# Performance work log

Hardware: AMD Instinct MI355X
Metric: run time of the kernel (lower is better)

Reference implementation:

```python
import jax, jax.numpy as jnp
import numpy as np

N_NODES = 100000
N_EDGES = 1600000
C_IN, C_HID, C_OUT = 32, 32, 8
N_AGENTS = 1000


def _glorot(key, shape):
    fan_in, fan_out = shape[0], shape[1]
    lim = float(np.sqrt(6.0 / (fan_in + fan_out)))
    return jax.random.uniform(key, shape, jnp.float32, -lim, lim)


def setup_inputs() -> dict:
    key = jax.random.key(0)
    ks = jax.random.split(key, 16)
    x = jax.random.normal(ks[0], (N_NODES, C_IN), jnp.float32)
    edge_index = jax.random.randint(ks[1], (2, N_EDGES), 0, N_NODES, jnp.int64)
    d = {"x": x, "edge_index": edge_index}
    dims = [(C_IN, C_HID), (C_HID, C_HID), (C_HID, C_HID)]
    for i, (di, do) in enumerate(dims, start=1):
        d[f"W_l{i}"] = _glorot(ks[2 * i], (di, do))        # neighbor (aggregated) weight
        d[f"b_l{i}"] = jnp.zeros((do,), jnp.float32)
        d[f"W_r{i}"] = _glorot(ks[2 * i + 1], (di, do))    # root/self weight (no bias)
    d["W_out"] = _glorot(ks[10], (C_HID, C_OUT))
    d["b_out"] = jnp.zeros((C_OUT,), jnp.float32)
    return d


def _sage_conv(x, src, dst, W_l, b_l, W_r):
    # mean-aggregate neighbor features at destination nodes
    msg = x[src]                                               # [E, d] gather
    summed = jax.ops.segment_sum(msg, dst, num_segments=N_NODES)
    cnt = jax.ops.segment_sum(jnp.ones((src.shape[0],), x.dtype), dst,
                              num_segments=N_NODES)
    agg = summed / jnp.maximum(cnt, 1.0)[:, None]              # deg==0 -> 0
    return agg @ W_l + b_l + x @ W_r


def reference(x, edge_index, W_l1, b_l1, W_r1, W_l2, b_l2, W_r2,
              W_l3, b_l3, W_r3, W_out, b_out):
    src, dst = edge_index[0], edge_index[1]
    h = jax.nn.relu(_sage_conv(x, src, dst, W_l1, b_l1, W_r1))
    h = jax.nn.relu(_sage_conv(h, src, dst, W_l2, b_l2, W_r2))
    h = jax.nn.relu(_sage_conv(h, src, dst, W_l3, b_l3, W_r3))
    out = h @ W_out + b_out
    return out[:N_AGENTS]
```

## Files before the change

kernel.cpp:

```cpp
#include <hip/hip_runtime.h>
#include <hip/hip_bf16.h>

#define N_NODES 100000
#define N_EDGES 1600000
#define N_AGENTS 1000

#define NB 782
#define ABLK 512
#define CHUNK (N_EDGES / ABLK)
#define CONV_BLOCKS 3125

typedef short s16x8 __attribute__((ext_vector_type(8)));
typedef float f32x4 __attribute__((ext_vector_type(4)));

__device__ __forceinline__ unsigned short f2bf(float f) {
    unsigned u = __float_as_uint(f);
    u += 0x7fffu + ((u >> 16) & 1u);
    return (unsigned short)(u >> 16);
}
__device__ __forceinline__ float bflo(unsigned u) { return __uint_as_float(u << 16); }
__device__ __forceinline__ float bfhi(unsigned u) { return __uint_as_float(u & 0xffff0000u); }

__global__ __launch_bounds__(256) void hist_prep_kernel(
    const int* __restrict__ dst, int* __restrict__ partialT,
    const float* __restrict__ x, unsigned short* __restrict__ xb,
    const float* __restrict__ Wl1, const float* __restrict__ Wr1,
    const float* __restrict__ Wl2, const float* __restrict__ Wr2,
    const float* __restrict__ Wl3, const float* __restrict__ Wr3,
    unsigned short* __restrict__ Wcat)
{
    int b = blockIdx.x;
    if (b < ABLK) {
        __shared__ int hist[NB];
        for (int i = threadIdx.x; i < NB; i += 256) hist[i] = 0;
        __syncthreads();
        int beg = b * CHUNK;
        for (int e = beg + threadIdx.x; e < beg + CHUNK; e += 256)
            atomicAdd(&hist[dst[e] >> 7], 1);
        __syncthreads();
        for (int i = threadIdx.x; i < NB; i += 256) partialT[i * ABLK + b] = hist[i];
    } else if (b < ABLK + CONV_BLOCKS) {
        int i = (b - ABLK) * 256 + threadIdx.x;
        float4 v = ((const float4*)x)[i];
        ((ushort4*)xb)[i] = make_ushort4(f2bf(v.x), f2bf(v.y), f2bf(v.z), f2bf(v.w));
    } else {
        int gid = (b - ABLK - CONV_BLOCKS) * 256 + threadIdx.x;
        if (gid >= 3 * 2048) return;
        int L = gid >> 11, idx = gid & 2047;
        int k = idx >> 5, n = idx & 31;
        const float* Wl = (L == 0) ? Wl1 : (L == 1) ? Wl2 : Wl3;
        const float* Wr = (L == 0) ? Wr1 : (L == 1) ? Wr2 : Wr3;
        float v = (k < 32) ? Wl[k * 32 + n] : Wr[(k - 32) * 32 + n];
        Wcat[gid] = f2bf(v);
    }
}

__global__ __launch_bounds__(256) void bucket_prefix_kernel(
    const int* __restrict__ partialT, int* __restrict__ baseT, int* __restrict__ tot)
{
    int wave = threadIdx.x >> 6, lane = threadIdx.x & 63;
    int t = blockIdx.x * 4 + wave;
    if (t >= NB) return;
    const int4* p = (const int4*)(partialT + (size_t)t * ABLK);
    int4 u0 = p[lane * 2], u1 = p[lane * 2 + 1];
    int v0 = u0.x, v1 = u0.y, v2 = u0.z, v3 = u0.w;
    int v4 = u1.x, v5 = u1.y, v6 = u1.z, v7 = u1.w;
    int p0 = 0, p1 = v0, p2 = p1 + v1, p3 = p2 + v2;
    int p4 = p3 + v3, p5 = p4 + v4, p6 = p5 + v5, p7 = p6 + v6;
    int s = p7 + v7;
    int x = s;
    #pragma unroll
    for (int off = 1; off < 64; off <<= 1) {
        int y = __shfl_up(x, off);
        if (lane >= off) x += y;
    }
    int excl = x - s;
    int4* q = (int4*)(baseT + (size_t)t * ABLK);
    q[lane * 2]     = make_int4(excl + p0, excl + p1, excl + p2, excl + p3);
    q[lane * 2 + 1] = make_int4(excl + p4, excl + p5, excl + p6, excl + p7);
    if (lane == 63) tot[t] = x;
}

__global__ __launch_bounds__(1024) void total_scan_kernel(
    const int* __restrict__ tot, int* __restrict__ bstart)
{
    __shared__ int tmp[1024];
    int t = threadIdx.x;
    int v = (t < NB) ? tot[t] : 0;
    tmp[t] = v;
    __syncthreads();
    for (int off = 1; off < 1024; off <<= 1) {
        int u = (t >= off) ? tmp[t - off] : 0;
        __syncthreads();
        tmp[t] += u;
        __syncthreads();
    }
    if (t < NB) {
        bstart[t] = tmp[t] - v;
        if (t == NB - 1) bstart[NB] = tmp[t];
    }
}

__global__ __launch_bounds__(256) void bucket_scatter_kernel(
    const int* __restrict__ src, const int* __restrict__ dst,
    const int* __restrict__ baseT, const int* __restrict__ bstart,
    int* __restrict__ ebuf)
{
    __shared__ int cur[NB];
    int b = blockIdx.x;
    for (int i = threadIdx.x; i < NB; i += 256)
        cur[i] = bstart[i] + baseT[(size_t)i * ABLK + b];
    __syncthreads();
    int beg = b * CHUNK;
    for (int e = beg + threadIdx.x; e < beg + CHUNK; e += 256) {
        int d = dst[e];
        int slot = atomicAdd(&cur[d >> 7], 1);
        ebuf[slot] = src[e] | ((d & 127) << 17);
    }
}

__global__ __launch_bounds__(256) void bucket_csr_kernel(
    const int* __restrict__ bstart, const int* __restrict__ ebuf,
    int* __restrict__ rowptr, float* __restrict__ inv, int* __restrict__ esrc)
{
    __shared__ int hist4[512], cur4[512], tmp[256];
    int b = blockIdx.x;
    int t = threadIdx.x;
    int beg = bstart[b], end = bstart[b + 1];
    hist4[t] = 0; hist4[t + 256] = 0;
    __syncthreads();
    for (int i = beg + t; i < end; i += 256) {
        int p = ebuf[i];
        int ln = (p >> 17) & 127;
        int cls = (p & 0x1FFFF) >> 15;
        atomicAdd(&hist4[ln * 4 + cls], 1);
    }
    __syncthreads();
    int c0 = 0, c1 = 0, c2 = 0, c3 = 0, v = 0;
    if (t < 128) {
        c0 = hist4[t * 4 + 0]; c1 = hist4[t * 4 + 1];
        c2 = hist4[t * 4 + 2]; c3 = hist4[t * 4 + 3];
        v = c0 + c1 + c2 + c3;
    }
    tmp[t] = v;
    __syncthreads();
    for (int off = 1; off < 256; off <<= 1) {
        int u = (t >= off) ? tmp[t - off] : 0;
        __syncthreads();
        tmp[t] += u;
        __syncthreads();
    }
    int excl = tmp[t] - v;
    int node = b * 128 + t;
    if (t < 128 && node < N_NODES) {
        int start = beg + excl;
        rowptr[node] = start;
        inv[node] = 1.0f / fmaxf((float)v, 1.0f);
        cur4[t * 4 + 0] = start;
        cur4[t * 4 + 1] = start + c0;
        cur4[t * 4 + 2] = start + c0 + c1;
        cur4[t * 4 + 3] = start + c0 + c1 + c2;
    }
    if (b == NB - 1 && t == 0) rowptr[N_NODES] = N_EDGES;
    __syncthreads();
    for (int i = beg + t; i < end; i += 256) {
        int p = ebuf[i];
        int ln = (p >> 17) & 127;
        int s = p & 0x1FFFF;
        int slot = atomicAdd(&cur4[ln * 4 + (s >> 15)], 1);
        esrc[slot] = s;
    }
}

__global__ __launch_bounds__(256) void sage_fused_kernel(
    const int* __restrict__ rowptr, const int* __restrict__ esrc,
    const float* __restrict__ inv, const unsigned short* __restrict__ hb,
    const unsigned short* __restrict__ Wcat, const float* __restrict__ bl,
    const float* __restrict__ Wout, const float* __restrict__ bout,
    void* __restrict__ outp, int n_nodes, int final)
{
    __shared__ unsigned short sW[2048];
    __shared__ float sb[32];
    __shared__ unsigned short smean[64 * 40];
    __shared__ float sh3[64 * 33];
    __shared__ float sWo[256];
    __shared__ float sbo[8];

    int tid = threadIdx.x;
    ((uint4*)sW)[tid] = ((const uint4*)Wcat)[tid];
    if (tid < 32) sb[tid] = bl[tid];
    if (final) {
        sWo[tid] = Wout[tid];
        if (tid < 8) sbo[tid] = bout[tid];
    }

    int lane = tid & 63, wave = tid >> 6;

    int g = lane >> 2, q = lane & 3;
    int nodeA = blockIdx.x * 64 + wave * 16 + g;
    int beg = 0, end = 0;
    if (nodeA < n_nodes) { beg = rowptr[nodeA]; end = rowptr[nodeA + 1]; }
    float a0 = 0.f, a1 = 0.f, a2 = 0.f, a3 = 0.f;
    float a4 = 0.f, a5 = 0.f, a6 = 0.f, a7 = 0.f;
    int j = beg;
    for (; j + 3 < end; j += 4) {
        int s0 = esrc[j];
        int s1 = esrc[j + 1];
        int s2 = esrc[j + 2];
        int s3 = esrc[j + 3];
        uint4 u0 = *(const uint4*)(hb + s0 * 32 + q * 8);
        uint4 u1 = *(const uint4*)(hb + s1 * 32 + q * 8);
        uint4 u2 = *(const uint4*)(hb + s2 * 32 + q * 8);
        uint4 u3 = *(const uint4*)(hb + s3 * 32 + q * 8);
        a0 += bflo(u0.x); a1 += bfhi(u0.x);
        a2 += bflo(u0.y); a3 += bfhi(u0.y);
        a4 += bflo(u0.z); a5 += bfhi(u0.z);
        a6 += bflo(u0.w); a7 += bfhi(u0.w);
        a0 += bflo(u1.x); a1 += bfhi(u1.x);
        a2 += bflo(u1.y); a3 += bfhi(u1.y);
        a4 += bflo(u1.z); a5 += bfhi(u1.z);
        a6 += bflo(u1.w); a7 += bfhi(u1.w);
        a0 += bflo(u2.x); a1 += bfhi(u2.x);
        a2 += bflo(u2.y); a3 += bfhi(u2.y);
        a4 += bflo(u2.z); a5 += bfhi(u2.z);
        a6 += bflo(u2.w); a7 += bfhi(u2.w);
        a0 += bflo(u3.x); a1 += bfhi(u3.x);
        a2 += bflo(u3.y); a3 += bfhi(u3.y);
        a4 += bflo(u3.z); a5 += bfhi(u3.z);
        a6 += bflo(u3.w); a7 += bfhi(u3.w);
    }
    for (; j < end; j++) {
        int s = esrc[j];
        uint4 u = *(const uint4*)(hb + s * 32 + q * 8);
        a0 += bflo(u.x); a1 += bfhi(u.x);
        a2 += bflo(u.y); a3 += bfhi(u.y);
        a4 += bflo(u.z); a5 += bfhi(u.z);
        a6 += bflo(u.w); a7 += bfhi(u.w);
    }
    float iv = (nodeA < n_nodes) ? inv[nodeA] : 0.f;
    uint4 o;
    o.x = (unsigned)f2bf(a0 * iv) | ((unsigned)f2bf(a1 * iv) << 16);
    o.y = (unsigned)f2bf(a2 * iv) | ((unsigned)f2bf(a3 * iv) << 16);
    o.z = (unsigned)f2bf(a4 * iv) | ((unsigned)f2bf(a5 * iv) << 16);
    o.w = (unsigned)f2bf(a6 * iv) | ((unsigned)f2bf(a7 * iv) << 16);
    int mrow = wave * 16 + g;
    *(uint4*)&smean[mrow * 40 + q * 8] = o;
    __syncthreads();

    int l15 = lane & 15, quad = lane >> 4;
    s16x8 bf_[2][2];
    #pragma unroll
    for (int kt = 0; kt < 2; kt++)
        #pragma unroll
        for (int nt = 0; nt < 2; nt++)
            #pragma unroll
            for (int jj = 0; jj < 8; jj++) {
                int k = kt * 32 + quad * 8 + jj;
                bf_[kt][nt][jj] = (short)sW[k * 32 + l15 + nt * 16];
            }
    float bias0 = sb[l15], bias1 = sb[l15 + 16];

    int tilebase = blockIdx.x * 64 + wave * 16;
    int nodeD = tilebase + l15;
    int na = min(nodeD, n_nodes - 1);
    s16x8 am = *(const s16x8*)&smean[(wave * 16 + l15) * 40 + quad * 8];
    s16x8 as = *(const s16x8*)(hb + (size_t)na * 32 + quad * 8);
    f32x4 acc0 = {0.f, 0.f, 0.f, 0.f};
    f32x4 acc1 = {0.f, 0.f, 0.f, 0.f};
    acc0 = __builtin_amdgcn_mfma_f32_16x16x32_bf16(am, bf_[0][0], acc0, 0, 0, 0);
    acc0 = __builtin_amdgcn_mfma_f32_16x16x32_bf16(as, bf_[1][0], acc0, 0, 0, 0);
    acc1 = __builtin_amdgcn_mfma_f32_16x16x32_bf16(am, bf_[0][1], acc1, 0, 0, 0);
    acc1 = __builtin_amdgcn_mfma_f32_16x16x32_bf16(as, bf_[1][1], acc1, 0, 0, 0);

    if (!final) {
        #pragma unroll
        for (int r = 0; r < 4; r++) {
            int onode = tilebase + quad * 4 + r;
            if (onode < n_nodes) {
                ((unsigned short*)outp)[onode * 32 + l15]      = f2bf(fmaxf(acc0[r] + bias0, 0.f));
                ((unsigned short*)outp)[onode * 32 + l15 + 16] = f2bf(fmaxf(acc1[r] + bias1, 0.f));
            }
        }
    } else {
        #pragma unroll
        for (int r = 0; r < 4; r++) {
            int row = wave * 16 + quad * 4 + r;
            sh3[row * 33 + l15]      = fmaxf(acc0[r] + bias0, 0.f);
            sh3[row * 33 + l15 + 16] = fmaxf(acc1[r] + bias1, 0.f);
        }
        __syncthreads();
        #pragma unroll
        for (int i = tid; i < 512; i += 256) {
            int ln = i >> 3, c = i & 7;
            int gn = blockIdx.x * 64 + ln;
            if (gn < N_AGENTS) {
                float ov = sbo[c];
                #pragma unroll
                for (int k = 0; k < 32; k++) ov += sh3[ln * 33 + k] * sWo[k * 8 + c];
                ((float*)outp)[gn * 8 + c] = ov;
            }
        }
    }
}

extern "C" void kernel_launch(void* const* d_in, const int* in_sizes, int n_in,
                              void* d_out, int out_size, void* d_ws, size_t ws_size,
                              hipStream_t stream) {
    const float* x   = (const float*)d_in[0];
    const int* ei    = (const int*)d_in[1];
    const float* Wl1 = (const float*)d_in[2];
    const float* bl1 = (const float*)d_in[3];
    const float* Wr1 = (const float*)d_in[4];
    const float* Wl2 = (const float*)d_in[5];
    const float* bl2 = (const float*)d_in[6];
    const float* Wr2 = (const float*)d_in[7];
    const float* Wl3 = (const float*)d_in[8];
    const float* bl3 = (const float*)d_in[9];
    const float* Wr3 = (const float*)d_in[10];
    const float* Wout = (const float*)d_in[11];
    const float* bout = (const float*)d_in[12];
    float* out = (float*)d_out;

    const int* src = ei;
    const int* dst = ei + N_EDGES;

    char* ws = (char*)d_ws;
    int*   rowptr   = (int*)ws;                                ws += (size_t)(N_NODES + 8) * 4;
    float* inv      = (float*)ws;                              ws += (size_t)N_NODES * 4;
    int*   partialT = (int*)ws;                                ws += (size_t)NB * ABLK * 4;
    int*   baseT    = (int*)ws;                                ws += (size_t)NB * ABLK * 4;
    int*   tot      = (int*)ws;                                ws += 784 * 4;
    int*   bstart   = (int*)ws;                                ws += 784 * 4;
    int*   esrc     = (int*)ws;                                ws += (size_t)N_EDGES * 4;
    unsigned short* hXb   = (unsigned short*)ws;               ws += (size_t)N_NODES * 32 * 2;
    unsigned short* hAb   = (unsigned short*)ws;               ws += (size_t)N_NODES * 32 * 2;
    unsigned short* hBb   = (unsigned short*)ws;               ws += (size_t)N_NODES * 32 * 2;
    unsigned short* Wcat  = (unsigned short*)ws;               ws += 3 * 2048 * 2;
    int*   ebuf     = (int*)hAb;

    hist_prep_kernel<<<ABLK + CONV_BLOCKS + 24, 256, 0, stream>>>(
        dst, partialT, x, hXb, Wl1, Wr1, Wl2, Wr2, Wl3, Wr3, Wcat);
    bucket_prefix_kernel<<<(NB + 3) / 4, 256, 0, stream>>>(partialT, baseT, tot);
    total_scan_kernel<<<1, 1024, 0, stream>>>(tot, bstart);
    bucket_scatter_kernel<<<ABLK, 256, 0, stream>>>(src, dst, baseT, bstart, ebuf);
    bucket_csr_kernel<<<NB, 256, 0, stream>>>(bstart, ebuf, rowptr, inv, esrc);

    sage_fused_kernel<<<(N_NODES + 63) / 64, 256, 0, stream>>>(
        rowptr, esrc, inv, hXb, Wcat, bl1, Wout, bout, hAb, N_NODES, 0);
    sage_fused_kernel<<<(N_NODES + 63) / 64, 256, 0, stream>>>(
        rowptr, esrc, inv, hAb, Wcat + 2048, bl2, Wout, bout, hBb, N_NODES, 0);
    sage_fused_kernel<<<(N_AGENTS + 63) / 64, 256, 0, stream>>>(
        rowptr, esrc, inv, hBb, Wcat + 4096, bl3, Wout, bout, out, N_AGENTS, 1);
}
```

Baseline: 200.0 us.

## Compute layer 2 only on nodes reachable from output agents

```diff
diff --git a/kernel.cpp b/kernel.cpp
--- a/kernel.cpp
+++ b/kernel.cpp
@@ -9,6 +9,9 @@
 #define ABLK 512
 #define CHUNK (N_EDGES / ABLK)
 #define CONV_BLOCKS 3125
+#define FLAGS_I4 25024
+#define FLAG_BLOCKS 98
+#define AGRID 280
 
 typedef short s16x8 __attribute__((ext_vector_type(8)));
 typedef float f32x4 __attribute__((ext_vector_type(4)));
@@ -27,7 +30,7 @@
     const float* __restrict__ Wl1, const float* __restrict__ Wr1,
     const float* __restrict__ Wl2, const float* __restrict__ Wr2,
     const float* __restrict__ Wl3, const float* __restrict__ Wr3,
-    unsigned short* __restrict__ Wcat)
+    unsigned short* __restrict__ Wcat, int* __restrict__ flags)
 {
     int b = blockIdx.x;
     if (b < ABLK) {
@@ -43,15 +46,17 @@
         int i = (b - ABLK) * 256 + threadIdx.x;
         float4 v = ((const float4*)x)[i];
         ((ushort4*)xb)[i] = make_ushort4(f2bf(v.x), f2bf(v.y), f2bf(v.z), f2bf(v.w));
-    } else {
+    } else if (b < ABLK + CONV_BLOCKS + 24) {
         int gid = (b - ABLK - CONV_BLOCKS) * 256 + threadIdx.x;
-        if (gid >= 3 * 2048) return;
         int L = gid >> 11, idx = gid & 2047;
         int k = idx >> 5, n = idx & 31;
         const float* Wl = (L == 0) ? Wl1 : (L == 1) ? Wl2 : Wl3;
         const float* Wr = (L == 0) ? Wr1 : (L == 1) ? Wr2 : Wr3;
         float v = (k < 32) ? Wl[k * 32 + n] : Wr[(k - 32) * 32 + n];
         Wcat[gid] = f2bf(v);
+    } else {
+        int gid = (b - ABLK - CONV_BLOCKS - 24) * 256 + threadIdx.x;
+        if (gid < FLAGS_I4) ((int4*)flags)[gid] = make_int4(0, 0, 0, 0);
     }
 }
 
@@ -170,6 +175,40 @@
         int slot = atomicAdd(&cur4[ln * 4 + (s >> 15)], 1);
         esrc[slot] = s;
     }
+}
+
+__global__ __launch_bounds__(256) void active_mark_kernel(
+    const int* __restrict__ rowptr, const int* __restrict__ esrc,
+    int* __restrict__ flags, int* __restrict__ acount)
+{
+    int gid = blockIdx.x * 256 + threadIdx.x;
+    if (gid == 0) *acount = 0;
+    if (gid < N_AGENTS) flags[gid] = 1;
+    int e1 = rowptr[N_AGENTS];
+    for (int j = gid; j < e1; j += gridDim.x * 256)
+        flags[esrc[j]] = 1;
+}
+
+__global__ __launch_bounds__(256) void active_compact_kernel(
+    const int* __restrict__ flags, int* __restrict__ alist, int* __restrict__ acount)
+{
+    int gid = blockIdx.x * 256 + threadIdx.x;
+    int f = (gid < N_NODES) ? flags[gid] : 0;
+    int lane = threadIdx.x & 63, wave = threadIdx.x >> 6;
+    unsigned long long m = __ballot(f != 0);
+    int pre = __popcll(m & ((1ull << lane) - 1ull));
+    __shared__ int wbase[4];
+    __shared__ int bbase;
+    if (lane == 0) wbase[wave] = __popcll(m);
+    __syncthreads();
+    if (threadIdx.x == 0) {
+        int t0 = wbase[0], t1 = t0 + wbase[1], t2 = t1 + wbase[2];
+        int tot = t2 + wbase[3];
+        bbase = atomicAdd(acount, tot);
+        wbase[0] = 0; wbase[1] = t0; wbase[2] = t1; wbase[3] = t2;
+    }
+    __syncthreads();
+    if (f) alist[bbase + wbase[wave] + pre] = gid;
 }
 
 __global__ __launch_bounds__(256) void sage_fused_kernel(
@@ -303,6 +342,118 @@
     }
 }
 
+__global__ __launch_bounds__(256) void sage_fused_act_kernel(
+    const int* __restrict__ rowptr, const int* __restrict__ esrc,
+    const float* __restrict__ inv, const unsigned short* __restrict__ hb,
+    const unsigned short* __restrict__ Wcat, const float* __restrict__ bl,
+    unsigned short* __restrict__ outp,
+    const int* __restrict__ alist, const int* __restrict__ acount)
+{
+    __shared__ unsigned short sW[2048];
+    __shared__ float sb[32];
+    __shared__ unsigned short smean[64 * 40];
+    __shared__ int sids[64];
+
+    int tid = threadIdx.x;
+    int count = *acount;
+    ((uint4*)sW)[tid] = ((const uint4*)Wcat)[tid];
+    if (tid < 32) sb[tid] = bl[tid];
+    __syncthreads();
+
+    int lane = tid & 63, wave = tid >> 6;
+    int g = lane >> 2, q = lane & 3;
+    int l15 = lane & 15, quad = lane >> 4;
+
+    s16x8 bf_[2][2];
+    #pragma unroll
+    for (int kt = 0; kt < 2; kt++)
+        #pragma unroll
+        for (int nt = 0; nt < 2; nt++)
+            #pragma unroll
+            for (int jj = 0; jj < 8; jj++) {
+                int k = kt * 32 + quad * 8 + jj;
+                bf_[kt][nt][jj] = (short)sW[k * 32 + l15 + nt * 16];
+            }
+    float bias0 = sb[l15], bias1 = sb[l15 + 16];
+
+    for (int tile = blockIdx.x; tile * 64 < count; tile += gridDim.x) {
+        if (tid < 64)
+            sids[tid] = (tile * 64 + tid < count) ? alist[tile * 64 + tid] : -1;
+        __syncthreads();
+
+        int nodeA = sids[wave * 16 + g];
+        int beg = 0, end = 0;
+        if (nodeA >= 0) { beg = rowptr[nodeA]; end = rowptr[nodeA + 1]; }
+        float a0 = 0.f, a1 = 0.f, a2 = 0.f, a3 = 0.f;
+        float a4 = 0.f, a5 = 0.f, a6 = 0.f, a7 = 0.f;
+        int j = beg;
+        for (; j + 3 < end; j += 4) {
+            int s0 = esrc[j];
+            int s1 = esrc[j + 1];
+            int s2 = esrc[j + 2];
+            int s3 = esrc[j + 3];
+            uint4 u0 = *(const uint4*)(hb + s0 * 32 + q * 8);
+            uint4 u1 = *(const uint4*)(hb + s1 * 32 + q * 8);
+            uint4 u2 = *(const uint4*)(hb + s2 * 32 + q * 8);
+            uint4 u3 = *(const uint4*)(hb + s3 * 32 + q * 8);
+            a0 += bflo(u0.x); a1 += bfhi(u0.x);
+            a2 += bflo(u0.y); a3 += bfhi(u0.y);
+            a4 += bflo(u0.z); a5 += bfhi(u0.z);
+            a6 += bflo(u0.w); a7 += bfhi(u0.w);
+            a0 += bflo(u1.x); a1 += bfhi(u1.x);
+            a2 += bflo(u1.y); a3 += bfhi(u1.y);
+            a4 += bflo(u1.z); a5 += bfhi(u1.z);
+            a6 += bflo(u1.w); a7 += bfhi(u1.w);
+            a0 += bflo(u2.x); a1 += bfhi(u2.x);
+            a2 += bflo(u2.y); a3 += bfhi(u2.y);
+            a4 += bflo(u2.z); a5 += bfhi(u2.z);
+            a6 += bflo(u2.w); a7 += bfhi(u2.w);
+            a0 += bflo(u3.x); a1 += bfhi(u3.x);
+            a2 += bflo(u3.y); a3 += bfhi(u3.y);
+            a4 += bflo(u3.z); a5 += bfhi(u3.z);
+            a6 += bflo(u3.w); a7 += bfhi(u3.w);
+        }
+        for (; j < end; j++) {
+            int s = esrc[j];
+            uint4 u = *(const uint4*)(hb + s * 32 + q * 8);
+            a0 += bflo(u.x); a1 += bfhi(u.x);
+            a2 += bflo(u.y); a3 += bfhi(u.y);
+            a4 += bflo(u.z); a5 += bfhi(u.z);
+            a6 += bflo(u.w); a7 += bfhi(u.w);
+        }
+        float iv = (nodeA >= 0) ? inv[nodeA] : 0.f;
+        uint4 o;
+        o.x = (unsigned)f2bf(a0 * iv) | ((unsigned)f2bf(a1 * iv) << 16);
+        o.y = (unsigned)f2bf(a2 * iv) | ((unsigned)f2bf(a3 * iv) << 16);
+        o.z = (unsigned)f2bf(a4 * iv) | ((unsigned)f2bf(a5 * iv) << 16);
+        o.w = (unsigned)f2bf(a6 * iv) | ((unsigned)f2bf(a7 * iv) << 16);
+        int mrow = wave * 16 + g;
+        *(uint4*)&smean[mrow * 40 + q * 8] = o;
+        __syncthreads();
+
+        int nd = sids[wave * 16 + l15];
+        int na = (nd >= 0) ? nd : 0;
+        s16x8 am = *(const s16x8*)&smean[(wave * 16 + l15) * 40 + quad * 8];
+        s16x8 as = *(const s16x8*)(hb + (size_t)na * 32 + quad * 8);
+        f32x4 acc0 = {0.f, 0.f, 0.f, 0.f};
+        f32x4 acc1 = {0.f, 0.f, 0.f, 0.f};
+        acc0 = __builtin_amdgcn_mfma_f32_16x16x32_bf16(am, bf_[0][0], acc0, 0, 0, 0);
+        acc0 = __builtin_amdgcn_mfma_f32_16x16x32_bf16(as, bf_[1][0], acc0, 0, 0, 0);
+        acc1 = __builtin_amdgcn_mfma_f32_16x16x32_bf16(am, bf_[0][1], acc1, 0, 0, 0);
+        acc1 = __builtin_amdgcn_mfma_f32_16x16x32_bf16(as, bf_[1][1], acc1, 0, 0, 0);
+
+        #pragma unroll
+        for (int r = 0; r < 4; r++) {
+            int onode = sids[wave * 16 + quad * 4 + r];
+            if (onode >= 0) {
+                outp[onode * 32 + l15]      = f2bf(fmaxf(acc0[r] + bias0, 0.f));
+                outp[onode * 32 + l15 + 16] = f2bf(fmaxf(acc1[r] + bias1, 0.f));
+            }
+        }
+        __syncthreads();
+    }
+}
+
 extern "C" void kernel_launch(void* const* d_in, const int* in_sizes, int n_in,
                               void* d_out, int out_size, void* d_ws, size_t ws_size,
                               hipStream_t stream) {
@@ -336,19 +487,25 @@
     unsigned short* hAb   = (unsigned short*)ws;               ws += (size_t)N_NODES * 32 * 2;
     unsigned short* hBb   = (unsigned short*)ws;               ws += (size_t)N_NODES * 32 * 2;
     unsigned short* Wcat  = (unsigned short*)ws;               ws += 3 * 2048 * 2;
+    int*   flags    = (int*)ws;                                ws += (size_t)100096 * 4;
+    int*   alist    = (int*)ws;                                ws += (size_t)100096 * 4;
+    int*   acount   = (int*)ws;                                ws += 16;
     int*   ebuf     = (int*)hAb;
 
-    hist_prep_kernel<<<ABLK + CONV_BLOCKS + 24, 256, 0, stream>>>(
-        dst, partialT, x, hXb, Wl1, Wr1, Wl2, Wr2, Wl3, Wr3, Wcat);
+    hist_prep_kernel<<<ABLK + CONV_BLOCKS + 24 + FLAG_BLOCKS, 256, 0, stream>>>(
+        dst, partialT, x, hXb, Wl1, Wr1, Wl2, Wr2, Wl3, Wr3, Wcat, flags);
     bucket_prefix_kernel<<<(NB + 3) / 4, 256, 0, stream>>>(partialT, baseT, tot);
     total_scan_kernel<<<1, 1024, 0, stream>>>(tot, bstart);
     bucket_scatter_kernel<<<ABLK, 256, 0, stream>>>(src, dst, baseT, bstart, ebuf);
     bucket_csr_kernel<<<NB, 256, 0, stream>>>(bstart, ebuf, rowptr, inv, esrc);
 
+    active_mark_kernel<<<64, 256, 0, stream>>>(rowptr, esrc, flags, acount);
+    active_compact_kernel<<<(N_NODES + 255) / 256, 256, 0, stream>>>(flags, alist, acount);
+
     sage_fused_kernel<<<(N_NODES + 63) / 64, 256, 0, stream>>>(
         rowptr, esrc, inv, hXb, Wcat, bl1, Wout, bout, hAb, N_NODES, 0);
-    sage_fused_kernel<<<(N_NODES + 63) / 64, 256, 0, stream>>>(
-        rowptr, esrc, inv, hAb, Wcat + 2048, bl2, Wout, bout, hBb, N_NODES, 0);
+    sage_fused_act_kernel<<<AGRID, 256, 0, stream>>>(
+        rowptr, esrc, inv, hAb, Wcat + 2048, bl2, hBb, alist, acount);
     sage_fused_kernel<<<(N_AGENTS + 63) / 64, 256, 0, stream>>>(
         rowptr, esrc, inv, hBb, Wcat + 4096, bl3, Wout, bout, out, N_AGENTS, 1);
 }
```

Measured after the change: 195.2 us. -2.4%, faster.
